# Kernel optimization log

Measured on AMD Instinct MI355X. Metric: run time of the kernel, lower is better.

The kernel has to match this reference:

```python
import jax, jax.numpy as jnp
import numpy as np

K = 4  # Chebyshev order (layer._k)

def setup_inputs() -> dict:
    key = jax.random.key(0)
    k1, k2, k3, k4 = jax.random.split(key, 4)
    N, din, dout = 4096, 128, 128
    a = jax.random.normal(k1, (N, din), dtype=jnp.float32)            # layer input (only len used)
    r = jax.random.uniform(k2, (N, dout), dtype=jnp.float32)          # upstream relevance (positive)
    # sparse-ish binary directed adjacency, no self loops (avg degree ~16)
    adj = (jax.random.uniform(k3, (N, N)) < (16.0 / N)).astype(jnp.float32)
    adj = adj * (1.0 - jnp.eye(N, dtype=jnp.float32))
    W = jax.random.normal(k4, (dout, K * din), dtype=jnp.float32) * 0.05  # ChebConv linear weight [out, K*in]
    return {"a": a, "r": r, "adj": adj, "W": W}

def _forward(a, r, adj, W):
    N = a.shape[0]
    dW = W.shape[1] // K
    # Wk[k] = W[:, k*dW:(k+1)*dW].T  -> [K, dimY(in), dimJ(out)]; rho = abs
    rhoW = jnp.abs(jnp.stack([W[:, k * dW:(k + 1) * dW].T for k in range(K)]))
    # Laplacian: L = I - D^{-1/2} A D^{-1/2}, degrees clamped at 1 (in-degrees = column sums)
    dinv = jnp.clip(adj.sum(axis=0), 1.0, None) ** -0.5
    D = dinv[:, None] * adj * dinv[None, :]
    L = jnp.eye(N, dtype=adj.dtype) - D
    # Chebyshev polynomials T_0=I, T_1=L, T_k = 2 L T_{k-1} - T_{k-2}  -> [K, N, N]
    Ts = [jnp.eye(N, dtype=L.dtype), L]
    for _ in range(2, K):
        Ts.append(2.0 * (L @ Ts[-1]) - Ts[-2])
    Ak = jnp.stack(Ts[:K])
    # U[i,j,x,y] = sum_k Ak[k,i,x] * rhoW[k,y,j]; never materialized.
    # denom[i,j] = U.sum(dim=(2,3)) = sum_k (sum_x Ak[k,i,x]) * (sum_y rhoW[k,y,j])
    denom = jnp.einsum('ki,kj->ij', Ak.sum(axis=2), rhoW.sum(axis=1))
    c = r / denom
    # out[x,y] = einsum('ijxy,ij->xy', U, c) = sum_k Ak[k].T @ c @ rhoW[k].T
    return jnp.einsum('kix,kyj,ij->xy', Ak, rhoW, c)

def reference(a, r, adj, W):
    return _forward(a, r, adj, W)
```

## Files before the change

kernel.cpp:

```cpp
#include <hip/hip_runtime.h>
#include <cstdint>
#include <cstddef>

#define N_NODES 4096
#define FEAT 128
#define KCH 4
#define NNZ_CAP (1 << 18)
#define TB2 256
#define TB3 256
#define T2CAP 2048
#define RSTRIDE 96

__device__ __forceinline__ int panel_of(int p) {
    return p < 3456 ? (p / 384) : (p < 3776 ? 9 : 10);
}

__global__ __launch_bounds__(256) void k_adj(const float* __restrict__ adj,
                                             int* __restrict__ deg,
                                             int* __restrict__ rdeg,
                                             int* __restrict__ rcolF) {
    int row = (blockIdx.x * 256 + threadIdx.x) >> 6;
    int lane = threadIdx.x & 63;
    const float* rowp = adj + (size_t)row * N_NODES;
    int base = 0;
    for (int it = 0; it < 64; ++it) {
        int x = it * 64 + lane;
        bool nz = rowp[x] != 0.0f;
        unsigned long long m = __ballot(nz);
        if (nz) {
            int idx = base + __popcll(m & ((1ull << lane) - 1ull));
            if (idx < RSTRIDE) rcolF[row * RSTRIDE + idx] = x;
            atomicAdd(&deg[x], 1);
        }
        base += __popcll(m);
    }
    if (lane == 0) rdeg[row] = (base > RSTRIDE) ? RSTRIDE : base;
}

__global__ __launch_bounds__(1024) void k_scan(const int* __restrict__ deg,
                                               float* __restrict__ dinv,
                                               int* __restrict__ colptr,
                                               int* __restrict__ colcur) {
    __shared__ int wsum[16];
    __shared__ int wbase[16];
    int t = threadIdx.x;
    int lane = t & 63, wv = t >> 6;
    int v[4]; int s = 0;
    for (int c = 0; c < 4; ++c) {
        int idx = t * 4 + c;
        int di = deg[idx];
        v[c] = di;
        s += di;
        float dc = fmaxf((float)di, 1.0f);
        dinv[idx] = (float)(1.0 / sqrt((double)dc));
    }
    int sc = s;
    for (int off = 1; off < 64; off <<= 1) {
        int n = __shfl_up(sc, off);
        if (lane >= off) sc += n;
    }
    if (lane == 63) wsum[wv] = sc;
    __syncthreads();
    if (t == 0) {
        int b = 0;
        for (int q2 = 0; q2 < 16; ++q2) { wbase[q2] = b; b += wsum[q2]; }
    }
    __syncthreads();
    int base = wbase[wv] + sc - s;
    for (int c = 0; c < 4; ++c) {
        int idx = t * 4 + c;
        colptr[idx] = base; colcur[idx] = base;
        base += v[c];
    }
    if (t == 1023) colptr[N_NODES] = base;
}

__global__ __launch_bounds__(256) void k_vals(const float* __restrict__ dinv,
                                              const int* __restrict__ rdeg,
                                              const int* __restrict__ rcolF,
                                              float* __restrict__ rlvalF,
                                              int* __restrict__ colcur,
                                              int* __restrict__ col_i,
                                              float* __restrict__ val,
                                              const float* __restrict__ W,
                                              float* __restrict__ sW) {
    if (blockIdx.x >= N_NODES / 4) {
        int tid = (blockIdx.x - N_NODES / 4) * 256 + threadIdx.x;
        int k = tid >> 7, j = tid & 127;
        float s = 0.f;
        for (int y = 0; y < FEAT; ++y)
            s += fabsf(W[(size_t)j * (KCH * FEAT) + k * FEAT + y]);
        sW[k * FEAT + j] = s;
        return;
    }
    int row = (blockIdx.x * 256 + threadIdx.x) >> 6;
    int lane = threadIdx.x & 63;
    int n = rdeg[row];
    float di = dinv[row];
    for (int e = lane; e < n; e += 64) {
        int x = rcolF[row * RSTRIDE + e];
        float dv = di * dinv[x];
        rlvalF[row * RSTRIDE + e] = -dv;
        int ec = atomicAdd(&colcur[x], 1);
        if (ec < NNZ_CAP) { col_i[ec] = row; val[ec] = dv; }
    }
}

__device__ __forceinline__ float np_pairwise_4096(const float* __restrict__ row,
                                                  float* r256, float* leaf,
                                                  float* bc, int t) {
    if (t < 256) {
        int L = t >> 3, j = t & 7;
        const float* p = row + L * 128 + j;
        float a = p[0];
        #pragma unroll
        for (int q = 1; q < 16; ++q) a += p[8 * q];
        r256[t] = a;
    }
    __syncthreads();
    if (t < 32) {
        const float* rr = r256 + t * 8;
        leaf[t] = ((rr[0] + rr[1]) + (rr[2] + rr[3])) + ((rr[4] + rr[5]) + (rr[6] + rr[7]));
    }
    __syncthreads();
    if (t == 0) {
        float v[32];
        #pragma unroll
        for (int q = 0; q < 32; ++q) v[q] = leaf[q];
        #pragma unroll
        for (int w = 16; w >= 1; w >>= 1)
            #pragma unroll
            for (int q = 0; q < 16; ++q)
                if (q < w) v[q] = v[2 * q] + v[2 * q + 1];
        bc[0] = v[0];
    }
    __syncthreads();
    float res = bc[0];
    __syncthreads();
    return res;
}

__global__ __launch_bounds__(TB2) void k_t2(const int* __restrict__ rdeg,
                                            const int* __restrict__ rcolF,
                                            const float* __restrict__ rlvalF,
                                            int2* __restrict__ t2sp,
                                            int* __restrict__ t2cnt,
                                            float* __restrict__ sA) {
    __shared__ float gp[N_NODES];
    __shared__ int   pcol[64];
    __shared__ float pLip[64];
    __shared__ int   pnn[64];
    __shared__ int   ssplit;
    __shared__ float r256[256], leaf[32], bc[1];
    __shared__ int   wtot[4], wbase[4];
    int t = threadIdx.x;
    int i = blockIdx.x;
    int rp = i * RSTRIDE;
    int ol = rdeg[i];
    int cnt = ol + 1;
    if (cnt > 64) cnt = 64;
    if (t == 0) ssplit = 0;
    __syncthreads();
    if (t < ol && rcolF[rp + t] < i) atomicAdd(&ssplit, 1);
    __syncthreads();
    int split = ssplit;
    if (t < cnt) {
        int col; float lip;
        if (t < split)       { col = rcolF[rp + t];     lip = rlvalF[rp + t]; }
        else if (t == split) { col = i;                 lip = 1.0f; }
        else                 { col = rcolF[rp + t - 1]; lip = rlvalF[rp + t - 1]; }
        pcol[t] = col; pLip[t] = lip; pnn[t] = rdeg[col];
    }
    float4* gp4 = (float4*)gp;
    const float4 z4 = make_float4(0.f, 0.f, 0.f, 0.f);
    #pragma unroll
    for (int u2 = 0; u2 < 4; ++u2) gp4[t + u2 * TB2] = z4;
    __syncthreads();
    for (int e = t; e < ol; e += TB2) gp[rcolF[rp + e]] = rlvalF[rp + e];
    if (t == 0) gp[i] = 1.0f;
    __syncthreads();
    float s1 = np_pairwise_4096(gp, r256, leaf, bc, t);
    for (int e = t; e < ol; e += TB2) gp[rcolF[rp + e]] = 0.0f;
    if (t == 0) gp[i] = 0.0f;
    __syncthreads();
    float tot[16];
    #pragma unroll
    for (int u = 0; u < 16; ++u) tot[u] = 0.0f;
    int q = 0;
    while (q < cnt) {
        {
            float lv = pLip[q];
            int p = pcol[q];
            int nn = pnn[q];
            int b = p * RSTRIDE;
            for (int e = t; e < nn; e += TB2)
                gp[rcolF[b + e]] = fmaf(lv, rlvalF[b + e], gp[rcolF[b + e]]);
            if (t == 0) gp[p] = fmaf(lv, 1.0f, gp[p]);
            __syncthreads();
        }
        ++q;
        if (q == cnt || panel_of(pcol[q]) != panel_of(pcol[q - 1])) {
            #pragma unroll
            for (int u2 = 0; u2 < 4; ++u2) {
                int idx = t + u2 * TB2;
                float4 b = gp4[idx];
                tot[4 * u2 + 0] = tot[4 * u2 + 0] + b.x;
                tot[4 * u2 + 1] = tot[4 * u2 + 1] + b.y;
                tot[4 * u2 + 2] = tot[4 * u2 + 2] + b.z;
                tot[4 * u2 + 3] = tot[4 * u2 + 3] + b.w;
                gp4[idx] = z4;
            }
            __syncthreads();
        }
    }
    #pragma unroll
    for (int u2 = 0; u2 < 4; ++u2) {
        int xb = 4 * t + 1024 * u2;
        float4 v;
        v.x = 2.0f * tot[4 * u2 + 0] - (xb + 0 == i ? 1.0f : 0.0f);
        v.y = 2.0f * tot[4 * u2 + 1] - (xb + 1 == i ? 1.0f : 0.0f);
        v.z = 2.0f * tot[4 * u2 + 2] - (xb + 2 == i ? 1.0f : 0.0f);
        v.w = 2.0f * tot[4 * u2 + 3] - (xb + 3 == i ? 1.0f : 0.0f);
        gp4[t + u2 * TB2] = v;
    }
    __syncthreads();
    float s2 = np_pairwise_4096(gp, r256, leaf, bc, t);
    float ev[16];
    #pragma unroll
    for (int u2 = 0; u2 < 4; ++u2) {
        float4 e4 = gp4[4 * t + u2];
        ev[4 * u2 + 0] = e4.x; ev[4 * u2 + 1] = e4.y;
        ev[4 * u2 + 2] = e4.z; ev[4 * u2 + 3] = e4.w;
    }
    int cl = 0;
    #pragma unroll
    for (int u = 0; u < 16; ++u) cl += (ev[u] != 0.0f);
    int lane = t & 63, wv = t >> 6;
    int sc = cl;
    for (int off = 1; off < 64; off <<= 1) {
        int n = __shfl_up(sc, off);
        if (lane >= off) sc += n;
    }
    if (lane == 63) wtot[wv] = sc;
    __syncthreads();
    if (t == 0) {
        int b = 0;
        for (int wq = 0; wq < 4; ++wq) { wbase[wq] = b; b += wtot[wq]; }
        t2cnt[i] = (b > T2CAP) ? T2CAP : b;
    }
    __syncthreads();
    int pos = wbase[wv] + sc - cl;
    int2* dst = t2sp + (size_t)i * T2CAP;
    #pragma unroll
    for (int u = 0; u < 16; ++u) {
        if (ev[u] != 0.0f) {
            if (pos < T2CAP) dst[pos] = make_int2(t * 16 + u, __float_as_int(ev[u]));
            ++pos;
        }
    }
    if (t == 0) {
        sA[0 * N_NODES + i] = 1.0f;
        sA[1 * N_NODES + i] = s1;
        sA[2 * N_NODES + i] = s2;
    }
}

__global__ __launch_bounds__(TB3) void k_t3(const int* __restrict__ rdeg,
                                            const int* __restrict__ rcolF,
                                            const float* __restrict__ rlvalF,
                                            const int2* __restrict__ t2sp,
                                            const int* __restrict__ t2cnt,
                                            float* __restrict__ sA) {
    __shared__ float gp[N_NODES];
    __shared__ int   pcol[64];
    __shared__ float pLip[64];
    __shared__ int   pnn[64];
    __shared__ int   ssplit;
    __shared__ float r256[256], leaf[32], bc[1];
    int t = threadIdx.x;
    int i = blockIdx.x;
    int rp = i * RSTRIDE;
    int ol = rdeg[i];
    int cnt = ol + 1;
    if (cnt > 64) cnt = 64;
    if (t == 0) ssplit = 0;
    __syncthreads();
    if (t < ol && rcolF[rp + t] < i) atomicAdd(&ssplit, 1);
    __syncthreads();
    int split = ssplit;
    if (t < cnt) {
        int col; float lip;
        if (t < split)       { col = rcolF[rp + t];     lip = rlvalF[rp + t]; }
        else if (t == split) { col = i;                  lip = 1.0f; }
        else                 { col = rcolF[rp + t - 1];  lip = rlvalF[rp + t - 1]; }
        pcol[t] = col; pLip[t] = lip; pnn[t] = t2cnt[col];
    }
    float4* gp4 = (float4*)gp;
    const float4 z4 = make_float4(0.f, 0.f, 0.f, 0.f);
    #pragma unroll
    for (int u2 = 0; u2 < 4; ++u2) gp4[t + u2 * TB3] = z4;
    __syncthreads();
    float tot[16];
    #pragma unroll
    for (int u = 0; u < 16; ++u) tot[u] = 0.0f;
    int q = 0;
    while (q < cnt) {
        {
            float lv = pLip[q];
            int nn = pnn[q];
            const int2* sp = t2sp + (size_t)pcol[q] * T2CAP;
            for (int e = t; e < nn; e += TB3) {
                int2 en = sp[e];
                gp[en.x] = fmaf(lv, __int_as_float(en.y), gp[en.x]);
            }
            __syncthreads();
        }
        ++q;
        if (q == cnt || panel_of(pcol[q]) != panel_of(pcol[q - 1])) {
            #pragma unroll
            for (int u2 = 0; u2 < 4; ++u2) {
                int idx = t + u2 * TB3;
                float4 b = gp4[idx];
                tot[4 * u2 + 0] = tot[4 * u2 + 0] + b.x;
                tot[4 * u2 + 1] = tot[4 * u2 + 1] + b.y;
                tot[4 * u2 + 2] = tot[4 * u2 + 2] + b.z;
                tot[4 * u2 + 3] = tot[4 * u2 + 3] + b.w;
                gp4[idx] = z4;
            }
            __syncthreads();
        }
    }
    #pragma unroll
    for (int u2 = 0; u2 < 4; ++u2) {
        float4 v;
        v.x = 2.0f * tot[4 * u2 + 0];
        v.y = 2.0f * tot[4 * u2 + 1];
        v.z = 2.0f * tot[4 * u2 + 2];
        v.w = 2.0f * tot[4 * u2 + 3];
        gp4[t + u2 * TB3] = v;
    }
    __syncthreads();
    for (int e = t; e < ol; e += TB3) { int x = rcolF[rp + e]; gp[x] = gp[x] - rlvalF[rp + e]; }
    if (t == 0) gp[i] = gp[i] - 1.0f;
    __syncthreads();
    float s3 = np_pairwise_4096(gp, r256, leaf, bc, t);
    if (t == 0) sA[3 * N_NODES + i] = s3;
}

__global__ __launch_bounds__(256) void k_cm(const float* __restrict__ r,
                                            const float* __restrict__ sA,
                                            const float* __restrict__ sW,
                                            const float* __restrict__ W,
                                            float* __restrict__ M) {
#pragma clang fp contract(off)
    __shared__ float cl[16][FEAT];
    int k = blockIdx.y;
    int ib = blockIdx.x * 16;
    int tx = threadIdx.x;
    int y = tx & 127, half = tx >> 7;
    for (int m = tx; m < 16 * FEAT; m += 256) {
        int i = ib + (m >> 7), j = m & 127;
        float denom = 0.0f;
        #pragma unroll
        for (int k2 = 0; k2 < KCH; ++k2) {
            float p = sA[k2 * N_NODES + i] * sW[k2 * FEAT + j];
            denom = denom + p;
        }
        cl[m >> 7][m & 127] = r[(size_t)i * FEAT + j] / denom;
    }
    __syncthreads();
    float acc[8];
    #pragma unroll
    for (int u = 0; u < 8; ++u) acc[u] = 0.0f;
    for (int j = 0; j < FEAT; ++j) {
        float a = fabsf(W[(size_t)j * (KCH * FEAT) + k * FEAT + y]);
        #pragma unroll
        for (int u = 0; u < 8; ++u) acc[u] += a * cl[half * 8 + u][j];
    }
    #pragma unroll
    for (int u = 0; u < 8; ++u)
        M[(size_t)k * N_NODES * FEAT + (size_t)(ib + half * 8 + u) * FEAT + y] = acc[u];
}

__global__ void k_h1(const int* __restrict__ colptr, const int* __restrict__ col_i,
                     const float* __restrict__ val, const float* __restrict__ M,
                     float* __restrict__ B2) {
    int x = blockIdx.x * 2 + (threadIdx.x >> 7);
    int y = threadIdx.x & 127;
    const float* M2 = M + (size_t)2 * N_NODES * FEAT;
    const float* M3 = M + (size_t)3 * N_NODES * FEAT;
    int e0 = colptr[x], e1 = colptr[x + 1];
    if (e1 > NNZ_CAP) e1 = NNZ_CAP;
    float g = 0.0f;
    for (int e = e0; e < e1; ++e)
        g += val[e] * M3[(size_t)col_i[e] * FEAT + y];
    size_t o = (size_t)x * FEAT + y;
    B2[o] = 2.0f * M2[o] + 4.0f * (M3[o] - g);
}

__global__ void k_h2(const int* __restrict__ colptr, const int* __restrict__ col_i,
                     const float* __restrict__ val, const float* __restrict__ M,
                     const float* __restrict__ B2, float* __restrict__ B3) {
    int x = blockIdx.x * 2 + (threadIdx.x >> 7);
    int y = threadIdx.x & 127;
    const float* M1 = M + (size_t)N_NODES * FEAT;
    const float* M3 = M + (size_t)3 * N_NODES * FEAT;
    int e0 = colptr[x], e1 = colptr[x + 1];
    if (e1 > NNZ_CAP) e1 = NNZ_CAP;
    float g = 0.0f;
    for (int e = e0; e < e1; ++e)
        g += val[e] * B2[(size_t)col_i[e] * FEAT + y];
    size_t o = (size_t)x * FEAT + y;
    B3[o] = (M1[o] - 3.0f * M3[o]) + (B2[o] - g);
}

__global__ void k_h3(const int* __restrict__ colptr, const int* __restrict__ col_i,
                     const float* __restrict__ val, const float* __restrict__ M,
                     const float* __restrict__ B3, float* __restrict__ out) {
    int x = blockIdx.x * 2 + (threadIdx.x >> 7);
    int y = threadIdx.x & 127;
    const float* M0 = M;
    const float* M2 = M + (size_t)2 * N_NODES * FEAT;
    int e0 = colptr[x], e1 = colptr[x + 1];
    if (e1 > NNZ_CAP) e1 = NNZ_CAP;
    float g = 0.0f;
    for (int e = e0; e < e1; ++e)
        g += val[e] * B3[(size_t)col_i[e] * FEAT + y];
    size_t o = (size_t)x * FEAT + y;
    out[o] = (M0[o] - M2[o]) + (B3[o] - g);
}

extern "C" void kernel_launch(void* const* d_in, const int* in_sizes, int n_in,
                              void* d_out, int out_size, void* d_ws, size_t ws_size,
                              hipStream_t stream) {
    const float* r   = (const float*)d_in[1];
    const float* adj = (const float*)d_in[2];
    const float* W   = (const float*)d_in[3];
    float* out = (float*)d_out;

    char* w = (char*)d_ws;
    auto take = [&](size_t bytes) {
        char* p = w;
        w += (bytes + 255) & ~(size_t)255;
        return p;
    };
    int*   deg    = (int*)take((size_t)N_NODES * 4);
    int*   rdeg   = (int*)take((size_t)N_NODES * 4);
    float* dinv   = (float*)take((size_t)N_NODES * 4);
    int*   colcur = (int*)take((size_t)N_NODES * 4);
    int*   colptr = (int*)take((size_t)(N_NODES + 1) * 4);
    int*   col_i  = (int*)take((size_t)NNZ_CAP * 4);
    float* val    = (float*)take((size_t)NNZ_CAP * 4);
    int*   rcolF  = (int*)take((size_t)N_NODES * RSTRIDE * 4);
    float* rlvalF = (float*)take((size_t)N_NODES * RSTRIDE * 4);
    float* sW     = (float*)take((size_t)KCH * FEAT * 4);
    float* sA     = (float*)take((size_t)KCH * N_NODES * 4);
    float* M      = (float*)take((size_t)KCH * N_NODES * FEAT * 4);
    float* B2     = (float*)take((size_t)N_NODES * FEAT * 4);
    float* B3     = (float*)take((size_t)N_NODES * FEAT * 4);
    int*   t2cnt  = (int*)take((size_t)N_NODES * 4);
    int2*  t2sp   = (int2*)take((size_t)N_NODES * T2CAP * 8);

    hipMemsetAsync(deg, 0, (size_t)N_NODES * 4, stream);
    k_adj<<<N_NODES / 4, 256, 0, stream>>>(adj, deg, rdeg, rcolF);
    k_scan<<<1, 1024, 0, stream>>>(deg, dinv, colptr, colcur);
    k_vals<<<N_NODES / 4 + 2, 256, 0, stream>>>(dinv, rdeg, rcolF, rlvalF,
                                                colcur, col_i, val, W, sW);
    k_t2<<<N_NODES, TB2, 0, stream>>>(rdeg, rcolF, rlvalF, t2sp, t2cnt, sA);
    k_t3<<<N_NODES, TB3, 0, stream>>>(rdeg, rcolF, rlvalF, t2sp, t2cnt, sA);
    k_cm<<<dim3(N_NODES / 16, KCH), 256, 0, stream>>>(r, sA, sW, W, M);
    k_h1<<<N_NODES / 2, 256, 0, stream>>>(colptr, col_i, val, M, B2);
    k_h2<<<N_NODES / 2, 256, 0, stream>>>(colptr, col_i, val, M, B2, B3);
    k_h3<<<N_NODES / 2, 256, 0, stream>>>(colptr, col_i, val, M, B3, out);
}
```

Baseline: 326.3 us.

## Vectorize adjacency scan with float4 loads and split T2 sparse storage into SoA

The adjacency scan now reads each row with float4 loads, replacing per-element ballots with a wavefront prefix scan over nibble counts, so there are fewer load instructions over the 64MB dense matrix. The sparse T2 rows are stored as separate 16-bit column and float value arrays instead of int2 pairs, which cuts the bytes written and gathered in k_t2/k_t3. The risk is the extra shuffle-scan cost per iteration and less coalesced per-lane stores for rcolF.

```diff
diff --git a/kernel.cpp b/kernel.cpp
--- a/kernel.cpp
+++ b/kernel.cpp
@@ -21,18 +21,29 @@
                                              int* __restrict__ rcolF) {
     int row = (blockIdx.x * 256 + threadIdx.x) >> 6;
     int lane = threadIdx.x & 63;
-    const float* rowp = adj + (size_t)row * N_NODES;
+    const float4* rowp = (const float4*)(adj + (size_t)row * N_NODES);
     int base = 0;
-    for (int it = 0; it < 64; ++it) {
-        int x = it * 64 + lane;
-        bool nz = rowp[x] != 0.0f;
-        unsigned long long m = __ballot(nz);
-        if (nz) {
-            int idx = base + __popcll(m & ((1ull << lane) - 1ull));
-            if (idx < RSTRIDE) rcolF[row * RSTRIDE + idx] = x;
-            atomicAdd(&deg[x], 1);
-        }
-        base += __popcll(m);
+    for (int it = 0; it < 16; ++it) {
+        float4 q = rowp[it * 64 + lane];
+        int nib = (q.x != 0.0f) | ((q.y != 0.0f) << 1)
+                | ((q.z != 0.0f) << 2) | ((q.w != 0.0f) << 3);
+        int cnt = __popc(nib);
+        int sc = cnt;
+        for (int off = 1; off < 64; off <<= 1) {
+            int n = __shfl_up(sc, off);
+            if (lane >= off) sc += n;
+        }
+        int myoff = base + sc - cnt;
+        int x0 = it * 256 + 4 * lane;
+        #pragma unroll
+        for (int c = 0; c < 4; ++c) {
+            if (nib & (1 << c)) {
+                if (myoff < RSTRIDE) rcolF[row * RSTRIDE + myoff] = x0 + c;
+                atomicAdd(&deg[x0 + c], 1);
+                ++myoff;
+            }
+        }
+        base += __shfl(sc, 63);
     }
     if (lane == 0) rdeg[row] = (base > RSTRIDE) ? RSTRIDE : base;
 }
@@ -143,7 +154,8 @@
 __global__ __launch_bounds__(TB2) void k_t2(const int* __restrict__ rdeg,
                                             const int* __restrict__ rcolF,
                                             const float* __restrict__ rlvalF,
-                                            int2* __restrict__ t2sp,
+                                            unsigned short* __restrict__ t2c,
+                                            float* __restrict__ t2v,
                                             int* __restrict__ t2cnt,
                                             float* __restrict__ sA) {
     __shared__ float gp[N_NODES];
@@ -250,11 +262,12 @@
     }
     __syncthreads();
     int pos = wbase[wv] + sc - cl;
-    int2* dst = t2sp + (size_t)i * T2CAP;
+    unsigned short* dstc = t2c + (size_t)i * T2CAP;
+    float* dstv = t2v + (size_t)i * T2CAP;
     #pragma unroll
     for (int u = 0; u < 16; ++u) {
         if (ev[u] != 0.0f) {
-            if (pos < T2CAP) dst[pos] = make_int2(t * 16 + u, __float_as_int(ev[u]));
+            if (pos < T2CAP) { dstc[pos] = (unsigned short)(t * 16 + u); dstv[pos] = ev[u]; }
             ++pos;
         }
     }
@@ -268,7 +281,8 @@
 __global__ __launch_bounds__(TB3) void k_t3(const int* __restrict__ rdeg,
                                             const int* __restrict__ rcolF,
                                             const float* __restrict__ rlvalF,
-                                            const int2* __restrict__ t2sp,
+                                            const unsigned short* __restrict__ t2c,
+                                            const float* __restrict__ t2v,
                                             const int* __restrict__ t2cnt,
                                             float* __restrict__ sA) {
     __shared__ float gp[N_NODES];
@@ -308,10 +322,11 @@
         {
             float lv = pLip[q];
             int nn = pnn[q];
-            const int2* sp = t2sp + (size_t)pcol[q] * T2CAP;
+            const unsigned short* spc = t2c + (size_t)pcol[q] * T2CAP;
+            const float* spv = t2v + (size_t)pcol[q] * T2CAP;
             for (int e = t; e < nn; e += TB3) {
-                int2 en = sp[e];
-                gp[en.x] = fmaf(lv, __int_as_float(en.y), gp[en.x]);
+                int x = spc[e];
+                gp[x] = fmaf(lv, spv[e], gp[x]);
             }
             __syncthreads();
         }
@@ -459,15 +474,16 @@
     float* B2     = (float*)take((size_t)N_NODES * FEAT * 4);
     float* B3     = (float*)take((size_t)N_NODES * FEAT * 4);
     int*   t2cnt  = (int*)take((size_t)N_NODES * 4);
-    int2*  t2sp   = (int2*)take((size_t)N_NODES * T2CAP * 8);
+    unsigned short* t2c = (unsigned short*)take((size_t)N_NODES * T2CAP * 2);
+    float* t2v    = (float*)take((size_t)N_NODES * T2CAP * 4);
 
     hipMemsetAsync(deg, 0, (size_t)N_NODES * 4, stream);
     k_adj<<<N_NODES / 4, 256, 0, stream>>>(adj, deg, rdeg, rcolF);
     k_scan<<<1, 1024, 0, stream>>>(deg, dinv, colptr, colcur);
     k_vals<<<N_NODES / 4 + 2, 256, 0, stream>>>(dinv, rdeg, rcolF, rlvalF,
                                                 colcur, col_i, val, W, sW);
-    k_t2<<<N_NODES, TB2, 0, stream>>>(rdeg, rcolF, rlvalF, t2sp, t2cnt, sA);
-    k_t3<<<N_NODES, TB3, 0, stream>>>(rdeg, rcolF, rlvalF, t2sp, t2cnt, sA);
+    k_t2<<<N_NODES, TB2, 0, stream>>>(rdeg, rcolF, rlvalF, t2c, t2v, t2cnt, sA);
+    k_t3<<<N_NODES, TB3, 0, stream>>>(rdeg, rcolF, rlvalF, t2c, t2v, t2cnt, sA);
     k_cm<<<dim3(N_NODES / 16, KCH), 256, 0, stream>>>(r, sA, sW, W, M);
     k_h1<<<N_NODES / 2, 256, 0, stream>>>(colptr, col_i, val, M, B2);
     k_h2<<<N_NODES / 2, 256, 0, stream>>>(colptr, col_i, val, M, B2, B3);
```

After: 306.6 us, median of 2. 1.06x faster.
